# Performance work log

Measured on AMD Instinct MI355X. Metric: run time of the kernel, lower is better.

## Reference

```python
import jax, jax.numpy as jnp
import numpy as np

EPS = 1e-9

def setup_inputs() -> dict:
    key = jax.random.key(0)
    k1, k2 = jax.random.split(key)
    B, N, D, E = 4, 4096, 2048, 64
    x = jax.random.normal(k1, (B, N, D), dtype=jnp.float32)
    w_gating = jax.random.normal(k2, (E, D), dtype=jnp.float32) * (1.0 / np.sqrt(D))
    return {"x": x, "w_gating": w_gating}

def reference(x, w_gating):
    # logits: [B, N, E] = x @ W^T  (nn.Linear, no bias)
    logits = jnp.einsum("bnd,ed->bne", x, w_gating)
    probs = jax.nn.softmax(logits, axis=-1)
    # top-2 selection; equivalent to argmax -> scatter(-inf) -> argmax chain
    top2_vals, top2_idx = jax.lax.top_k(probs, 2)  # [B, N, 2]
    denom = top2_vals[..., 0] + top2_vals[..., 1] + EPS
    combine_weights = top2_vals / denom[..., None]  # [B, N, 2]
    expert_index = top2_idx.astype(jnp.int32)       # [B, N, 2]
    return combine_weights, expert_index
```

## Files before the change

kernel.cpp:

```cpp
#include <hip/hip_runtime.h>
#include <math.h>

#define K_DIM 2048
#define E_DIM 64
#define BM 32
#define NW 4
#define KW (K_DIM / NW)
#define KS 32
#define NSTEP (KW / KS)
#define WSCALE 64.0f

typedef _Float16 f16x8 __attribute__((ext_vector_type(8)));
typedef float    f32x4 __attribute__((ext_vector_type(4)));

__global__ void pack_w_kernel(const float* __restrict__ w, _Float16* __restrict__ wpk) {
    int tid  = (int)blockIdx.x * 256 + (int)threadIdx.x;
    int lane = tid & 63;
    int n    = (tid >> 6) & 3;
    int kk   = tid >> 8;
    int col  = n * 16 + (lane & 15);
    int k    = kk * 32 + (lane >> 4) * 8;
    const float* src = w + (size_t)col * K_DIM + k;
    _Float16* hi = wpk + (size_t)tid * 8;
    _Float16* lo = hi + (size_t)K_DIM * E_DIM;
    #pragma unroll
    for (int j = 0; j < 8; ++j) {
        float v = src[j] * WSCALE;
        _Float16 h = (_Float16)v;
        hi[j] = h;
        lo[j] = (_Float16)(v - (float)h);
    }
}

template<int PACKED>
__global__ __launch_bounds__(256, 2) void mfma_gate_kernel(
    const float* __restrict__ x,
    const float* __restrict__ w,
    const _Float16* __restrict__ wpk,
    float* __restrict__ out, int M)
{
    __shared__ float red[NW][BM][E_DIM + 1];

    const int t    = (int)threadIdx.x;
    const int lane = t & 63;
    const int wave = __builtin_amdgcn_readfirstlane(t >> 6);
    const int lr   = lane & 15;
    const int ks   = lane >> 4;
    const int rowbase = (int)blockIdx.x * BM;
    const size_t k0 = (size_t)wave * KW;

    f32x4 acc[2][4];
    #pragma unroll
    for (int m = 0; m < 2; ++m)
        #pragma unroll
        for (int n = 0; n < 4; ++n)
            acc[m][n] = (f32x4){0.f, 0.f, 0.f, 0.f};

    const float* xa = x + (size_t)(rowbase + lr) * K_DIM + k0 + (size_t)ks * 8;
    const _Float16* wph = wpk + ((size_t)(wave * NSTEP) * 4 * 64 + lane) * 8;
    const _Float16* wpl = wph + (size_t)K_DIM * E_DIM;

    for (int s = 0; s < NSTEP; ++s) {
        f16x8 ah[2], al[2];
        #pragma unroll
        for (int m = 0; m < 2; ++m) {
            const float* p = xa + (size_t)m * 16 * K_DIM + (size_t)s * KS;
            float4 u0 = *(const float4*)p;
            float4 u1 = *(const float4*)(p + 4);
            float uu[8] = {u0.x, u0.y, u0.z, u0.w, u1.x, u1.y, u1.z, u1.w};
            #pragma unroll
            for (int j = 0; j < 8; ++j) {
                _Float16 h = (_Float16)uu[j];
                ah[m][j] = h;
                al[m][j] = (_Float16)(uu[j] - (float)h);
            }
        }
        f16x8 bh[4], bl[4];
        if (PACKED) {
            #pragma unroll
            for (int n = 0; n < 4; ++n) {
                bh[n] = *(const f16x8*)(wph + ((size_t)s * 4 + n) * 64 * 8);
                bl[n] = *(const f16x8*)(wpl + ((size_t)s * 4 + n) * 64 * 8);
            }
        } else {
            #pragma unroll
            for (int n = 0; n < 4; ++n) {
                const float* p = w + (size_t)(n * 16 + lr) * K_DIM + k0 + (size_t)s * KS + (size_t)ks * 8;
                float4 u0 = *(const float4*)p;
                float4 u1 = *(const float4*)(p + 4);
                float uu[8] = {u0.x, u0.y, u0.z, u0.w, u1.x, u1.y, u1.z, u1.w};
                #pragma unroll
                for (int j = 0; j < 8; ++j) {
                    float v = uu[j] * WSCALE;
                    _Float16 h = (_Float16)v;
                    bh[n][j] = h;
                    bl[n][j] = (_Float16)(v - (float)h);
                }
            }
        }
        #pragma unroll
        for (int m = 0; m < 2; ++m)
            #pragma unroll
            for (int n = 0; n < 4; ++n) {
                acc[m][n] = __builtin_amdgcn_mfma_f32_16x16x32_f16(ah[m], bh[n], acc[m][n], 0, 0, 0);
                acc[m][n] = __builtin_amdgcn_mfma_f32_16x16x32_f16(ah[m], bl[n], acc[m][n], 0, 0, 0);
                acc[m][n] = __builtin_amdgcn_mfma_f32_16x16x32_f16(al[m], bh[n], acc[m][n], 0, 0, 0);
            }
    }

    const float inv = 1.0f / WSCALE;
    #pragma unroll
    for (int m = 0; m < 2; ++m)
        #pragma unroll
        for (int n = 0; n < 4; ++n)
            #pragma unroll
            for (int j = 0; j < 4; ++j)
                red[wave][m * 16 + ks * 4 + j][n * 16 + lr] = acc[m][n][j] * inv;
    __syncthreads();

    #pragma unroll 1
    for (int rr = 0; rr < BM / NW; ++rr) {
        const int r = wave * (BM / NW) + rr;
        float l = red[0][r][lane] + red[1][r][lane] + red[2][r][lane] + red[3][r][lane];

        float m = l;
        #pragma unroll
        for (int off = 32; off >= 1; off >>= 1)
            m = fmaxf(m, __shfl_xor(m, off));

        float e = expf(l - m);
        float z = e;
        #pragma unroll
        for (int off = 32; off >= 1; off >>= 1)
            z += __shfl_xor(z, off);
        const float p = e / z;

        float v1 = p; int i1 = lane;
        #pragma unroll
        for (int off = 32; off >= 1; off >>= 1) {
            float ov = __shfl_xor(v1, off);
            int   oi = __shfl_xor(i1, off);
            if (ov > v1 || (ov == v1 && oi < i1)) { v1 = ov; i1 = oi; }
        }

        float v2 = (lane == i1) ? -1.0f : p; int i2 = lane;
        #pragma unroll
        for (int off = 32; off >= 1; off >>= 1) {
            float ov = __shfl_xor(v2, off);
            int   oi = __shfl_xor(i2, off);
            if (ov > v2 || (ov == v2 && oi < i2)) { v2 = ov; i2 = oi; }
        }

        if (lane == 0) {
            const size_t row = (size_t)rowbase + r;
            const float denom = v1 + v2 + 1e-9f;
            out[row * 2 + 0] = v1 / denom;
            out[row * 2 + 1] = v2 / denom;
            out[(size_t)M * 2 + row * 2 + 0] = (float)i1;
            out[(size_t)M * 2 + row * 2 + 1] = (float)i2;
        }
    }
}

extern "C" void kernel_launch(void* const* d_in, const int* in_sizes, int n_in,
                              void* d_out, int out_size, void* d_ws, size_t ws_size,
                              hipStream_t stream)
{
    const float* x = (const float*)d_in[0];
    const float* w = (const float*)d_in[1];
    float* out = (float*)d_out;
    const int M = in_sizes[0] / K_DIM;
    const int grid = M / BM;

    const size_t pack_bytes = (size_t)K_DIM * E_DIM * 2 * sizeof(_Float16);
    if (ws_size >= pack_bytes) {
        pack_w_kernel<<<64, 256, 0, stream>>>(w, (_Float16*)d_ws);
        mfma_gate_kernel<1><<<grid, 256, 0, stream>>>(x, w, (const _Float16*)d_ws, out, M);
    } else {
        mfma_gate_kernel<0><<<grid, 256, 0, stream>>>(x, w, nullptr, out, M);
    }
}
```

Before: 47.49 us.

## Halve row tile, raise occupancy, and software-prefetch x across k-steps

Reduces the block row tile from 32 to 16 rows, which doubles the grid and allows four blocks per CU through the launch bounds. Adds register double-buffering of the next x chunk so its global load overlaps the current step's MFMAs, and changes the reduction-buffer padding. The cost is that each packed weight fragment is now reused across only one 16-row tile instead of two, doubling weight traffic per row. The prefetch wraps around and issues one redundant in-bounds load on the last iteration.

```diff
diff --git a/kernel.cpp b/kernel.cpp
--- a/kernel.cpp
+++ b/kernel.cpp
@@ -3,12 +3,13 @@
 
 #define K_DIM 2048
 #define E_DIM 64
-#define BM 32
+#define BM 16
 #define NW 4
 #define KW (K_DIM / NW)
 #define KS 32
 #define NSTEP (KW / KS)
 #define WSCALE 64.0f
+#define RSTRIDE (E_DIM + 4)
 
 typedef _Float16 f16x8 __attribute__((ext_vector_type(8)));
 typedef float    f32x4 __attribute__((ext_vector_type(4)));
@@ -33,13 +34,13 @@
 }
 
 template<int PACKED>
-__global__ __launch_bounds__(256, 2) void mfma_gate_kernel(
+__global__ __launch_bounds__(256, 4) void mfma_gate_kernel(
     const float* __restrict__ x,
     const float* __restrict__ w,
     const _Float16* __restrict__ wpk,
     float* __restrict__ out, int M)
 {
-    __shared__ float red[NW][BM][E_DIM + 1];
+    __shared__ float red[NW][BM][RSTRIDE];
 
     const int t    = (int)threadIdx.x;
     const int lane = t & 63;
@@ -49,32 +50,24 @@
     const int rowbase = (int)blockIdx.x * BM;
     const size_t k0 = (size_t)wave * KW;
 
-    f32x4 acc[2][4];
+    f32x4 acc[4];
     #pragma unroll
-    for (int m = 0; m < 2; ++m)
-        #pragma unroll
-        for (int n = 0; n < 4; ++n)
-            acc[m][n] = (f32x4){0.f, 0.f, 0.f, 0.f};
+    for (int n = 0; n < 4; ++n)
+        acc[n] = (f32x4){0.f, 0.f, 0.f, 0.f};
 
     const float* xa = x + (size_t)(rowbase + lr) * K_DIM + k0 + (size_t)ks * 8;
     const _Float16* wph = wpk + ((size_t)(wave * NSTEP) * 4 * 64 + lane) * 8;
     const _Float16* wpl = wph + (size_t)K_DIM * E_DIM;
 
+    float4 c0 = *(const float4*)(xa);
+    float4 c1 = *(const float4*)(xa + 4);
+
+    #pragma unroll 2
     for (int s = 0; s < NSTEP; ++s) {
-        f16x8 ah[2], al[2];
-        #pragma unroll
-        for (int m = 0; m < 2; ++m) {
-            const float* p = xa + (size_t)m * 16 * K_DIM + (size_t)s * KS;
-            float4 u0 = *(const float4*)p;
-            float4 u1 = *(const float4*)(p + 4);
-            float uu[8] = {u0.x, u0.y, u0.z, u0.w, u1.x, u1.y, u1.z, u1.w};
-            #pragma unroll
-            for (int j = 0; j < 8; ++j) {
-                _Float16 h = (_Float16)uu[j];
-                ah[m][j] = h;
-                al[m][j] = (_Float16)(uu[j] - (float)h);
-            }
-        }
+        const int sn = (s + 1) & (NSTEP - 1);
+        float4 n0 = *(const float4*)(xa + sn * KS);
+        float4 n1 = *(const float4*)(xa + sn * KS + 4);
+
         f16x8 bh[4], bl[4];
         if (PACKED) {
             #pragma unroll
@@ -98,24 +91,34 @@
                 }
             }
         }
+
+        f16x8 ah, al;
+        {
+            float u[8] = {c0.x, c0.y, c0.z, c0.w, c1.x, c1.y, c1.z, c1.w};
+            #pragma unroll
+            for (int j = 0; j < 8; ++j) {
+                _Float16 h = (_Float16)u[j];
+                ah[j] = h;
+                al[j] = (_Float16)(u[j] - (float)h);
+            }
+        }
+
         #pragma unroll
-        for (int m = 0; m < 2; ++m)
-            #pragma unroll
-            for (int n = 0; n < 4; ++n) {
-                acc[m][n] = __builtin_amdgcn_mfma_f32_16x16x32_f16(ah[m], bh[n], acc[m][n], 0, 0, 0);
-                acc[m][n] = __builtin_amdgcn_mfma_f32_16x16x32_f16(ah[m], bl[n], acc[m][n], 0, 0, 0);
-                acc[m][n] = __builtin_amdgcn_mfma_f32_16x16x32_f16(al[m], bh[n], acc[m][n], 0, 0, 0);
-            }
+        for (int n = 0; n < 4; ++n) {
+            acc[n] = __builtin_amdgcn_mfma_f32_16x16x32_f16(ah, bh[n], acc[n], 0, 0, 0);
+            acc[n] = __builtin_amdgcn_mfma_f32_16x16x32_f16(ah, bl[n], acc[n], 0, 0, 0);
+            acc[n] = __builtin_amdgcn_mfma_f32_16x16x32_f16(al, bh[n], acc[n], 0, 0, 0);
+        }
+
+        c0 = n0; c1 = n1;
     }
 
     const float inv = 1.0f / WSCALE;
     #pragma unroll
-    for (int m = 0; m < 2; ++m)
+    for (int n = 0; n < 4; ++n)
         #pragma unroll
-        for (int n = 0; n < 4; ++n)
-            #pragma unroll
-            for (int j = 0; j < 4; ++j)
-                red[wave][m * 16 + ks * 4 + j][n * 16 + lr] = acc[m][n][j] * inv;
+        for (int j = 0; j < 4; ++j)
+            red[wave][ks * 4 + j][n * 16 + lr] = acc[n][j] * inv;
     __syncthreads();
 
     #pragma unroll 1
```

New measurement: 51.82 us. +9.1%, slower.
